# Performance work log

Measured on AMD Instinct MI355X. Metric: run time of the kernel, lower is better.

Reference implementation:

```python
import jax, jax.numpy as jnp
import numpy as np

TAU = 1.0

def setup_inputs() -> dict:
    key = jax.random.key(0)
    k1, k2 = jax.random.split(key)
    x = jax.random.uniform(k1, (1, 8192), dtype=jnp.float32)
    weight = jax.random.uniform(k2, (8192, 8192), dtype=jnp.float32)  # uniform_(0,1) init
    t = 128
    return {"x": x, "weight": weight, "t": t}

def reference(x, weight, t):
    # x = x / max(x) * 255 ; x = floor(x / tau)
    xq = jnp.floor((x / jnp.max(x)) * 255.0 / TAU)
    # spike mask: int32(t) == int32(x[0][i]) per element, vectorized
    spikes = (xq[0].astype(jnp.int32) == jnp.int32(t)).astype(weight.dtype)  # [in_features]
    # broadcast multiply: [out_features, in_features] * [in_features]
    return weight * spikes
```

## Files before the change

### kernel.cpp

```cpp
#include <hip/hip_runtime.h>

#define N_COLS 8192

__global__ __launch_bounds__(1024) void spike_kernel(const float* __restrict__ x,
                                                     const int* __restrict__ t_ptr,
                                                     float* __restrict__ spikes) {
    __shared__ float smax[16];
    __shared__ float s_maxv;
    const int tid = threadIdx.x;

    float vals[8];
    float m = -1e30f;
#pragma unroll
    for (int j = 0; j < 8; ++j) {
        vals[j] = x[tid + j * 1024];
        m = fmaxf(m, vals[j]);
    }
#pragma unroll
    for (int off = 32; off > 0; off >>= 1)
        m = fmaxf(m, __shfl_down(m, off, 64));
    if ((tid & 63) == 0) smax[tid >> 6] = m;
    __syncthreads();
    if (tid < 16) {
        float mm = smax[tid];
#pragma unroll
        for (int off = 8; off > 0; off >>= 1)
            mm = fmaxf(mm, __shfl_down(mm, off, 16));
        if (tid == 0) s_maxv = mm;
    }
    __syncthreads();

    const float maxv = s_maxv;
    const int t = *t_ptr;
#pragma unroll
    for (int j = 0; j < 8; ++j) {
        const int q = (int)floorf((vals[j] / maxv) * 255.0f);
        spikes[tid + j * 1024] = (q == t) ? 1.0f : 0.0f;
    }
}

__global__ __launch_bounds__(256) void mul_kernel(const float4* __restrict__ w,
                                                  const float* __restrict__ spikes,
                                                  float4* __restrict__ out) {
    const unsigned int i = blockIdx.x * blockDim.x + threadIdx.x;
    const unsigned int col = (i * 4u) & (N_COLS - 1);
    const float4 s = *(const float4*)(spikes + col);
    float4 o;
    if (s.x == 0.0f && s.y == 0.0f && s.z == 0.0f && s.w == 0.0f) {
        o = make_float4(0.0f, 0.0f, 0.0f, 0.0f);
    } else {
        const float4 wv = w[i];
        o = make_float4(wv.x * s.x, wv.y * s.y, wv.z * s.z, wv.w * s.w);
    }
    out[i] = o;
}

extern "C" void kernel_launch(void* const* d_in, const int* in_sizes, int n_in,
                              void* d_out, int out_size, void* d_ws, size_t ws_size,
                              hipStream_t stream) {
    const float* x = (const float*)d_in[0];
    const float4* w = (const float4*)d_in[1];
    const int* t = (const int*)d_in[2];
    float* out = (float*)d_out;
    float* spikes = (float*)d_ws;

    spike_kernel<<<1, 1024, 0, stream>>>(x, t, spikes);

    const int n4 = out_size / 4;
    mul_kernel<<<n4 / 256, 256, 0, stream>>>(w, spikes, (float4*)out);
}
```

Baseline: 419.8 us.

## Compact spiking columns and scatter weights over a memset output

The spike kernel now writes a compact list of columns that match t, along with their count, instead of a dense spike mask. The output is zeroed with hipMemsetAsync, and a grid-stride scatter kernel then copies only the weight entries in those columns. This is meant to replace the per-float4 mask check and full output write with a memset plus a small sparse copy. The cost is an extra memset launch and strided, uncoalesced column reads and writes, which perform poorly if many columns spike.

```diff
diff --git a/kernel.cpp b/kernel.cpp
--- a/kernel.cpp
+++ b/kernel.cpp
@@ -1,13 +1,17 @@
 #include <hip/hip_runtime.h>
 
 #define N_COLS 8192
+#define LOG2_COLS 13
 
 __global__ __launch_bounds__(1024) void spike_kernel(const float* __restrict__ x,
                                                      const int* __restrict__ t_ptr,
-                                                     float* __restrict__ spikes) {
+                                                     int* __restrict__ meta) {
     __shared__ float smax[16];
     __shared__ float s_maxv;
+    __shared__ int s_count;
     const int tid = threadIdx.x;
+
+    if (tid == 0) s_count = 0;
 
     float vals[8];
     float m = -1e30f;
@@ -35,37 +39,43 @@
 #pragma unroll
     for (int j = 0; j < 8; ++j) {
         const int q = (int)floorf((vals[j] / maxv) * 255.0f);
-        spikes[tid + j * 1024] = (q == t) ? 1.0f : 0.0f;
+        if (q == t) {
+            const int slot = atomicAdd(&s_count, 1);
+            meta[1 + slot] = tid + j * 1024;
+        }
     }
+    __syncthreads();
+    if (tid == 0) meta[0] = s_count;
 }
 
-__global__ __launch_bounds__(256) void mul_kernel(const float4* __restrict__ w,
-                                                  const float* __restrict__ spikes,
-                                                  float4* __restrict__ out) {
-    const unsigned int i = blockIdx.x * blockDim.x + threadIdx.x;
-    const unsigned int col = (i * 4u) & (N_COLS - 1);
-    const float4 s = *(const float4*)(spikes + col);
-    float4 o;
-    if (s.x == 0.0f && s.y == 0.0f && s.z == 0.0f && s.w == 0.0f) {
-        o = make_float4(0.0f, 0.0f, 0.0f, 0.0f);
-    } else {
-        const float4 wv = w[i];
-        o = make_float4(wv.x * s.x, wv.y * s.y, wv.z * s.z, wv.w * s.w);
+__global__ __launch_bounds__(256) void scatter_kernel(const float* __restrict__ w,
+                                                      const int* __restrict__ meta,
+                                                      float* __restrict__ out) {
+    const int count = meta[0];
+    const int* cols = meta + 1;
+    const long total = (long)count << LOG2_COLS;
+    const long stride = (long)gridDim.x * blockDim.x;
+    for (long idx = (long)blockIdx.x * blockDim.x + threadIdx.x; idx < total;
+         idx += stride) {
+        const int k = (int)(idx >> LOG2_COLS);
+        const int r = (int)(idx & (N_COLS - 1));
+        const long off = ((long)r << LOG2_COLS) + cols[k];
+        out[off] = w[off];
     }
-    out[i] = o;
 }
 
 extern "C" void kernel_launch(void* const* d_in, const int* in_sizes, int n_in,
                               void* d_out, int out_size, void* d_ws, size_t ws_size,
                               hipStream_t stream) {
     const float* x = (const float*)d_in[0];
-    const float4* w = (const float4*)d_in[1];
+    const float* w = (const float*)d_in[1];
     const int* t = (const int*)d_in[2];
     float* out = (float*)d_out;
-    float* spikes = (float*)d_ws;
+    int* meta = (int*)d_ws;
 
-    spike_kernel<<<1, 1024, 0, stream>>>(x, t, spikes);
+    spike_kernel<<<1, 1024, 0, stream>>>(x, t, meta);
 
-    const int n4 = out_size / 4;
-    mul_kernel<<<n4 / 256, 256, 0, stream>>>(w, spikes, (float4*)out);
+    hipMemsetAsync(out, 0, (size_t)out_size * sizeof(float), stream);
+
+    scatter_kernel<<<2048, 256, 0, stream>>>(w, meta, out);
 }
```

After: 414.0 us. Within noise of the previous version (-1.4%).
